# Optimization experiments

Measured on AMD Instinct MI355X. Metric: run time of the kernel, lower is better.

The kernel has to match this reference:

```python
import jax, jax.numpy as jnp
import numpy as np
import math

H = 4          # n_heads
LAM = 2.0      # gate_lambda
EPS = 1e-6


def _evid_gate(t, W, b):
    # t: [B,T,d] -> g: [B,T,1] via Normal-Inverse-Gamma evidential gate
    h = t @ W.T + b                                  # [B,T,4]
    mu, v_raw, a_raw, b_raw = jnp.split(h, 4, axis=-1)
    v = jax.nn.softplus(v_raw) + EPS
    alpha = jax.nn.softplus(a_raw) + 1.0 + EPS
    beta = jax.nn.softplus(b_raw) + EPS
    var_ep = beta / (v * (alpha - 1.0))
    g = jax.nn.sigmoid(mu) * jnp.exp(-LAM * var_ep)
    return jnp.maximum(g, 1e-6)


def _ln(t, g, b):
    m = jnp.mean(t, axis=-1, keepdims=True)
    v = jnp.var(t, axis=-1, keepdims=True)
    return (t - m) / jnp.sqrt(v + 1e-5) * g + b


def _split(t):
    B, T, d = t.shape
    return t.reshape(B, T, H, d // H).transpose(0, 2, 1, 3)  # [B,H,T,dk]


def _merge(t):
    B, h, T, dk = t.shape
    return t.transpose(0, 2, 1, 3).reshape(B, T, h * dk)


def _gated_attn(q, k, v, lg_q, lg_k, mask_k, dk):
    # q:[B,H,Tq,dk], k/v:[B,H,Tk,dk], lg_q:[B,Tq], lg_k:[B,Tk], mask_k:[B,Tk] bool
    s = jnp.einsum('bhqd,bhkd->bhqk', q, k) / math.sqrt(dk)
    s = s + lg_q[:, None, :, None] + lg_k[:, None, None, :]
    s = jnp.where(mask_k[:, None, None, :], s, -jnp.inf)
    a = jax.nn.softmax(s, axis=-1)                   # dropout is identity in eval
    return jnp.einsum('bhqk,bhkd->bhqd', a, v)


def setup_inputs():
    key = jax.random.key(0)
    ks = jax.random.split(key, 20)
    B, Nx, Ny, d = 16, 512, 1024, 256
    s = 0.02
    w = lambda k, shape: jax.random.normal(k, shape, jnp.float32) * s
    return {
        'x': jax.random.normal(ks[0], (B, Nx, d), jnp.float32),
        'y': jax.random.normal(ks[1], (B, Ny, d), jnp.float32),
        'x_mask': jnp.ones((B, Nx), bool),
        'y_mask': jnp.ones((B, Ny), bool),
        'Wqx': w(ks[2], (d, d)), 'Wkx': w(ks[3], (d, d)), 'Wvx': w(ks[4], (d, d)),
        'Wqy': w(ks[5], (d, d)), 'Wky': w(ks[6], (d, d)), 'Wvy': w(ks[7], (d, d)),
        'gWx': w(ks[8], (4, d)), 'gbx': jnp.zeros((4,), jnp.float32),
        'gWy': w(ks[9], (4, d)), 'gby': jnp.zeros((4,), jnp.float32),
        'Wox': w(ks[10], (d, d)), 'Woy': w(ks[11], (d, d)),
        'lnx_g': jnp.ones((d,), jnp.float32), 'lnx_b': jnp.zeros((d,), jnp.float32),
        'lny_g': jnp.ones((d,), jnp.float32), 'lny_b': jnp.zeros((d,), jnp.float32),
        'ffx_W': w(ks[12], (d, d)), 'ffx_b': jnp.zeros((d,), jnp.float32),
        'ffy_W': w(ks[13], (d, d)), 'ffy_b': jnp.zeros((d,), jnp.float32),
    }


def reference(x, y, x_mask, y_mask, Wqx, Wkx, Wvx, Wqy, Wky, Wvy,
              gWx, gbx, gWy, gby, Wox, Woy,
              lnx_g, lnx_b, lny_g, lny_b, ffx_W, ffx_b, ffy_W, ffy_b):
    d = x.shape[-1]
    dk = d // H
    qx, kx, vx = _split(x @ Wqx.T), _split(x @ Wkx.T), _split(x @ Wvx.T)
    qy, ky, vy = _split(y @ Wqy.T), _split(y @ Wky.T), _split(y @ Wvy.T)
    gx = _evid_gate(x, gWx, gbx)                     # [B,Nx,1]
    gy = _evid_gate(y, gWy, gby)                     # [B,Ny,1]
    lgx = jnp.log(gx)[..., 0]                        # [B,Nx]
    lgy = jnp.log(gy)[..., 0]                        # [B,Ny]

    out_x = _merge(_gated_attn(qx, ky, vy, lgx, lgy, y_mask, dk)) @ Wox.T
    x2 = _ln(x + out_x, lnx_g, lnx_b)
    x2 = _ln(x2 + jax.nn.silu(x2 @ ffx_W.T + ffx_b), lnx_g, lnx_b)

    out_y = _merge(_gated_attn(qy, kx, vx, lgy, lgx, x_mask, dk)) @ Woy.T
    y2 = _ln(y + out_y, lny_g, lny_b)
    y2 = _ln(y2 + jax.nn.silu(y2 @ ffy_W.T + ffy_b), lny_g, lny_b)

    return x2, y2, gx[..., 0], gy[..., 0]
```

## Files before the change

kernel.cpp:

```cpp
#include <hip/hip_runtime.h>
#include <stdint.h>

typedef unsigned short u16;
typedef unsigned int   u32;
typedef __attribute__((ext_vector_type(8))) short bf16x8;
typedef __attribute__((ext_vector_type(4))) float f32x4;

__device__ __forceinline__ u16 f2b(float f) {
    union { float f; u32 i; } v; v.f = f;
    return (u16)((v.i + 0x7fffu + ((v.i >> 16) & 1u)) >> 16);
}
__device__ __forceinline__ float b2f(u16 u) {
    union { float f; u32 i; } v; v.i = ((u32)u) << 16; return v.f;
}
__device__ __forceinline__ bf16x8 pack8(const float* s) {
    union { bf16x8 v; u16 u[8]; } r;
    #pragma unroll
    for (int i = 0; i < 8; i++) r.u[i] = f2b(s[i]);
    return r.v;
}
__device__ __forceinline__ float softplus_f(float x) {
    return x > 15.f ? x : log1pf(__expf(x));
}

__global__ __launch_bounds__(256) void prep(
    const float* __restrict__ X, const float* __restrict__ Y,
    const float* __restrict__ gWx, const float* __restrict__ gbx,
    const float* __restrict__ gWy, const float* __restrict__ gby,
    float* __restrict__ goutx, float* __restrict__ lgx,
    float* __restrict__ gouty, float* __restrict__ lgy,
    u16* __restrict__ xb, u16* __restrict__ yb,
    const float* p0, const float* p1, const float* p2, const float* p3,
    const float* p4, const float* p5, const float* p6, const float* p7,
    const float* p8, const float* p9, u16* __restrict__ wdst)
{
    const int blk = blockIdx.x;
    const int t = threadIdx.x;
    if (blk < 3072) {
        int g = blk * 256 + t;
        const bool isx = g < 262144;
        const float* src; u16* dst; size_t off; int tok;
        const float *gW, *gb; float *go, *lg;
        if (isx) {
            src = X; dst = xb; off = (size_t)g * 8; tok = g >> 5;
            gW = gWx; gb = gbx; go = goutx; lg = lgx;
        } else {
            int g2 = g - 262144;
            src = Y; dst = yb; off = (size_t)g2 * 8; tok = g2 >> 5;
            gW = gWy; gb = gby; go = gouty; lg = lgy;
        }
        float tmp[8];
        *(float4*)&tmp[0] = *(const float4*)(src + off);
        *(float4*)&tmp[4] = *(const float4*)(src + off + 4);
        *(bf16x8*)(dst + off) = pack8(tmp);

        const int c0 = (t & 31) * 8;
        float a[4];
        #pragma unroll
        for (int j = 0; j < 4; j++) {
            float4 w0 = *(const float4*)(gW + j * 256 + c0);
            float4 w1 = *(const float4*)(gW + j * 256 + c0 + 4);
            a[j] = tmp[0]*w0.x + tmp[1]*w0.y + tmp[2]*w0.z + tmp[3]*w0.w
                 + tmp[4]*w1.x + tmp[5]*w1.y + tmp[6]*w1.z + tmp[7]*w1.w;
        }
        #pragma unroll
        for (int o = 16; o > 0; o >>= 1) {
            #pragma unroll
            for (int j = 0; j < 4; j++) a[j] += __shfl_xor(a[j], o);
        }
        if ((t & 31) == 0) {
            float mu    = a[0] + gb[0];
            float v     = softplus_f(a[1] + gb[1]) + 1e-6f;
            float alpha = softplus_f(a[2] + gb[2]) + 1.0f + 1e-6f;
            float beta  = softplus_f(a[3] + gb[3]) + 1e-6f;
            float var_ep = beta / (v * (alpha - 1.0f));
            float sig = 1.0f / (1.0f + __expf(-mu));
            float gg = fmaxf(sig * __expf(-2.0f * var_ep), 1e-6f);
            go[tok] = gg;
            lg[tok] = log2f(gg);
        }
    } else {
        int g = (blk - 3072) * 256 + t;
        int wsel = g >> 13, off = g & 8191;
        const float* src;
        switch (wsel) {
            case 0: src = p0; break; case 1: src = p1; break;
            case 2: src = p2; break; case 3: src = p3; break;
            case 4: src = p4; break; case 5: src = p5; break;
            case 6: src = p6; break; case 7: src = p7; break;
            case 8: src = p8; break; default: src = p9; break;
        }
        float tmp[8];
        *(float4*)&tmp[0] = *(const float4*)(src + (size_t)off * 8);
        *(float4*)&tmp[4] = *(const float4*)(src + (size_t)off * 8 + 4);
        *(bf16x8*)(wdst + ((size_t)wsel * 65536) + (size_t)off * 8) = pack8(tmp);
    }
}

__global__ __launch_bounds__(256, 2) void gemm_qkv(
    const u16* __restrict__ Axb, const u16* __restrict__ Ayb,
    const u16* __restrict__ Wx, const u16* __restrict__ Wy,
    u16* __restrict__ Qx, u16* __restrict__ Kx, u16* __restrict__ VTx,
    u16* __restrict__ Qy, u16* __restrict__ Ky, u16* __restrict__ VTy)
{
    __shared__ short smem[2 * 128 * 72];
    short* As = smem;
    short* Ws = smem + 128 * 72;
    const int t = threadIdx.x;
    const int id = blockIdx.x;
    const int wk = (id & 7) * 144 + (id >> 3);
    const int bn = wk % 6;
    int bm = wk / 6;
    const bool isx = bm < 64;
    const u16* A  = isx ? Axb : Ayb;
    const u16* W  = isx ? Wx : Wy;
    u16* Qo  = isx ? Qx : Qy;
    u16* Ko  = isx ? Kx : Ky;
    u16* VTo = isx ? VTx : VTy;
    const int tqsh = isx ? 9 : 10;
    if (!isx) bm -= 64;

    const int w = t >> 6, lane = t & 63, li = lane & 15, quad = lane >> 4;
    const int wm = (w >> 1) * 64, wn = (w & 1) * 64;
    const int sr = t >> 1, scb = (t & 1) * 32;

    f32x4 zero = {0.f, 0.f, 0.f, 0.f};
    f32x4 acc[4][4];
    #pragma unroll
    for (int a = 0; a < 4; a++)
        #pragma unroll
        for (int b = 0; b < 4; b++) acc[a][b] = zero;

    for (int ch = 0; ch < 4; ch++) {
        const int k0 = ch * 64;
        if (ch) __syncthreads();
        {
            const u16* Ap = A + (size_t)(bm * 128 + sr) * 256 + k0 + scb;
            const u16* Wp = W + (size_t)(bn * 128 + sr) * 256 + k0 + scb;
            #pragma unroll
            for (int j = 0; j < 4; j++) {
                *(uint4*)&As[sr * 72 + scb + j * 8] = *(const uint4*)(Ap + j * 8);
                *(uint4*)&Ws[sr * 72 + scb + j * 8] = *(const uint4*)(Wp + j * 8);
            }
        }
        __syncthreads();
        #pragma unroll
        for (int c = 0; c < 2; c++) {
            bf16x8 af[4], bf[4];
            #pragma unroll
            for (int mt = 0; mt < 4; mt++)
                af[mt] = *(const bf16x8*)&As[(wm + mt * 16 + li) * 72 + c * 32 + quad * 8];
            #pragma unroll
            for (int nt = 0; nt < 4; nt++)
                bf[nt] = *(const bf16x8*)&Ws[(wn + nt * 16 + li) * 72 + c * 32 + quad * 8];
            #pragma unroll
            for (int mt = 0; mt < 4; mt++)
                #pragma unroll
                for (int nt = 0; nt < 4; nt++)
                    acc[mt][nt] = __builtin_amdgcn_mfma_f32_16x16x32_bf16(
                        af[mt], bf[nt], acc[mt][nt], 0, 0, 0);
        }
    }

    const int sel = bn >> 1;
    if (sel < 2) {
        u16* Co = (sel == 0) ? Qo : Ko;
        #pragma unroll
        for (int nt = 0; nt < 4; nt++) {
            const int c = (bn * 128 + wn + nt * 16 + li) & 255;
            #pragma unroll
            for (int mt = 0; mt < 4; mt++) {
                const int row0 = bm * 128 + wm + mt * 16 + quad * 4;
                #pragma unroll
                for (int i = 0; i < 4; i++)
                    Co[(size_t)(row0 + i) * 256 + c] = f2b(acc[mt][nt][i]);
            }
        }
    } else {
        __syncthreads();
        short* Trans = smem;
        #pragma unroll
        for (int nt = 0; nt < 4; nt++) {
            const int cl = wn + nt * 16 + li;
            #pragma unroll
            for (int mt = 0; mt < 4; mt++) {
                const int rl0 = wm + mt * 16 + quad * 4;
                #pragma unroll
                for (int i = 0; i < 4; i++)
                    Trans[cl * 136 + rl0 + i] = (short)f2b(acc[mt][nt][i]);
            }
        }
        __syncthreads();
        const int dl = t >> 1, seg = t & 1;
        const int col = (bn - 4) * 128 + dl;
        const int h = col >> 6, dd = col & 63;
        const int bz = (bm * 128) >> tqsh;
        const int key0 = (bm * 128) & ((1 << tqsh) - 1);
        u16* dst = VTo + ((((size_t)(bz * 4 + h)) * 64 + dd) << tqsh) + key0 + seg * 64;
        #pragma unroll
        for (int k = 0; k < 8; k++)
            *(uint4*)(dst + k * 8) = *(const uint4*)&Trans[dl * 136 + seg * 64 + k * 8];
    }
}

__global__ __launch_bounds__(256, 3) void attn3(
    const u16* __restrict__ Q1, const u16* __restrict__ K1, const u16* __restrict__ VT1,
    const float* __restrict__ LG1, u16* __restrict__ O1,
    const u16* __restrict__ Q2, const u16* __restrict__ K2, const u16* __restrict__ VT2,
    const float* __restrict__ LG2, u16* __restrict__ O2)
{
    __shared__ short Ks[64][72];
    __shared__ short VTs[64][72];
    __shared__ short Ps[128][72];
    __shared__ float Lk[64];

    const int t = threadIdx.x;
    const int id = blockIdx.x;
    const int wk = (id & 7) * 96 + (id >> 3);
    const int xi = wk % 12;
    const int rest = wk / 12;
    const int h = rest & 3;
    const int bz = rest >> 2;
    const bool ph1 = xi < 4;
    const int qtl = ph1 ? xi : xi - 4;
    const u16* Q  = ph1 ? Q1 : Q2;
    const u16* K  = ph1 ? K1 : K2;
    const u16* VT = ph1 ? VT1 : VT2;
    const float* LG = ph1 ? LG1 : LG2;
    u16* O = ph1 ? O1 : O2;
    const int Tq = ph1 ? 512 : 1024;
    const int Tk = ph1 ? 1024 : 512;

    const int w = t >> 6, lane = t & 63, li = lane & 15, quad = lane >> 4;
    const int q0 = qtl * 128;

    bf16x8 qf[2][2];
    #pragma unroll
    for (int s = 0; s < 2; s++) {
        const u16* qp = Q + (size_t)(bz * Tq + q0 + s * 64 + w * 16 + li) * 256 + h * 64 + quad * 8;
        qf[s][0] = *(const bf16x8*)qp;
        qf[s][1] = *(const bf16x8*)(qp + 32);
    }

    float lsum[2] = {0.f, 0.f};
    f32x4 zero = {0.f, 0.f, 0.f, 0.f};
    f32x4 oacc[2][4];
    #pragma unroll
    for (int s = 0; s < 2; s++)
        #pragma unroll
        for (int md = 0; md < 4; md++) oacc[s][md] = zero;

    const int sr = t >> 2, sc = (t & 3) * 16;
    const u16* Kp  = K + (size_t)(bz * Tk + sr) * 256 + h * 64 + sc;
    const u16* VTp = VT + ((size_t)(bz * 4 + h) * 64 + sr) * Tk + sc;
    const float* LGp = LG + (size_t)bz * Tk;

    uint4 pk0, pk1, pv0, pv1;
    float plk;
    pk0 = *(const uint4*)(Kp);
    pk1 = *(const uint4*)(Kp + 8);
    pv0 = *(const uint4*)(VTp);
    pv1 = *(const uint4*)(VTp + 8);
    plk = (t < 64) ? LGp[t] : 0.f;

    const float SCL = 0.18033688f;

    for (int kt = 0; kt < Tk; kt += 64) {
        __syncthreads();
        *(uint4*)&Ks[sr][sc]      = pk0;
        *(uint4*)&Ks[sr][sc + 8]  = pk1;
        *(uint4*)&VTs[sr][sc]     = pv0;
        *(uint4*)&VTs[sr][sc + 8] = pv1;
        if (t < 64) Lk[t] = plk;
        __syncthreads();
        if (kt + 64 < Tk) {
            pk0 = *(const uint4*)(Kp + (size_t)(kt + 64) * 256);
            pk1 = *(const uint4*)(Kp + (size_t)(kt + 64) * 256 + 8);
            pv0 = *(const uint4*)(VTp + kt + 64);
            pv1 = *(const uint4*)(VTp + kt + 64 + 8);
            if (t < 64) plk = LGp[kt + 64 + t];
        }

        #pragma unroll
        for (int s = 0; s < 2; s++) {
            f32x4 sacc[4] = {zero, zero, zero, zero};
            #pragma unroll
            for (int c = 0; c < 2; c++)
                #pragma unroll
                for (int mt = 0; mt < 4; mt++) {
                    bf16x8 af = *(const bf16x8*)&Ks[mt * 16 + li][c * 32 + quad * 8];
                    sacc[mt] = __builtin_amdgcn_mfma_f32_16x16x32_bf16(af, qf[s][c], sacc[mt], 0, 0, 0);
                }
            #pragma unroll
            for (int mt = 0; mt < 4; mt++) {
                float4 lk4 = *(const float4*)&Lk[mt * 16 + quad * 4];
                float x0 = fmaf(sacc[mt][0], SCL, lk4.x);
                float x1 = fmaf(sacc[mt][1], SCL, lk4.y);
                float x2 = fmaf(sacc[mt][2], SCL, lk4.z);
                float x3 = fmaf(sacc[mt][3], SCL, lk4.w);
                float p0, p1, p2, p3;
                asm("v_exp_f32 %0, %1" : "=v"(p0) : "v"(x0));
                asm("v_exp_f32 %0, %1" : "=v"(p1) : "v"(x1));
                asm("v_exp_f32 %0, %1" : "=v"(p2) : "v"(x2));
                asm("v_exp_f32 %0, %1" : "=v"(p3) : "v"(x3));
                lsum[s] += (p0 + p1) + (p2 + p3);
                u32 lo, hi;
                asm("v_cvt_pk_bf16_f32 %0, %1, %2" : "=v"(lo) : "v"(p0), "v"(p1));
                asm("v_cvt_pk_bf16_f32 %0, %1, %2" : "=v"(hi) : "v"(p2), "v"(p3));
                uint2 st; st.x = lo; st.y = hi;
                *(uint2*)&Ps[s * 64 + w * 16 + li][mt * 16 + quad * 4] = st;
            }
        }

        #pragma unroll
        for (int c = 0; c < 2; c++) {
            bf16x8 vf[4], pf[2];
            #pragma unroll
            for (int md = 0; md < 4; md++)
                vf[md] = *(const bf16x8*)&VTs[md * 16 + li][c * 32 + quad * 8];
            #pragma unroll
            for (int s = 0; s < 2; s++)
                pf[s] = *(const bf16x8*)&Ps[s * 64 + w * 16 + li][c * 32 + quad * 8];
            #pragma unroll
            for (int s = 0; s < 2; s++)
                #pragma unroll
                for (int md = 0; md < 4; md++)
                    oacc[s][md] = __builtin_amdgcn_mfma_f32_16x16x32_bf16(
                        vf[md], pf[s], oacc[s][md], 0, 0, 0);
        }
    }

    #pragma unroll
    for (int s = 0; s < 2; s++) {
        float l = lsum[s];
        l += __shfl_xor(l, 16);
        l += __shfl_xor(l, 32);
        const float inv = 1.0f / l;
        u16* op = O + (size_t)(bz * Tq + q0 + s * 64 + w * 16 + li) * 256 + h * 64;
        #pragma unroll
        for (int md = 0; md < 4; md++) {
            float o0 = oacc[s][md][0] * inv;
            float o1 = oacc[s][md][1] * inv;
            float o2 = oacc[s][md][2] * inv;
            float o3 = oacc[s][md][3] * inv;
            u32 lo, hi;
            asm("v_cvt_pk_bf16_f32 %0, %1, %2" : "=v"(lo) : "v"(o0), "v"(o1));
            asm("v_cvt_pk_bf16_f32 %0, %1, %2" : "=v"(hi) : "v"(o2), "v"(o3));
            uint2 st; st.x = lo; st.y = hi;
            *(uint2*)(op + md * 16 + quad * 4) = st;
        }
    }
}

template<int ACT>
__global__ __launch_bounds__(256, 3) void gemm_ln(
    const u16* __restrict__ Axb, const u16* __restrict__ Ayb,
    const u16* __restrict__ Wxb, const u16* __restrict__ Wyb,
    const float* __restrict__ bx, const float* __restrict__ by,
    const float* __restrict__ Rx, const float* __restrict__ Ry,
    const float* __restrict__ gxv, const float* __restrict__ bxv,
    const float* __restrict__ gyv, const float* __restrict__ byv,
    float* __restrict__ Fx, float* __restrict__ Fy,
    u16* __restrict__ Bx, u16* __restrict__ By)
{
    __shared__ short As[32 * 72];
    __shared__ short Ws[256 * 72];
    __shared__ float Sred[32][4];
    __shared__ float Ssq[32][4];

    const int t = threadIdx.x;
    int blk = blockIdx.x;
    const bool isx = blk < 256;
    const u16* A = isx ? Axb : Ayb;
    const u16* W = isx ? Wxb : Wyb;
    const float* bias  = isx ? bx : by;
    const float* RES   = isx ? Rx : Ry;
    const float* gamma = isx ? gxv : gyv;
    const float* beta  = isx ? bxv : byv;
    float* F = isx ? Fx : Fy;
    u16*   B = isx ? Bx : By;
    if (!isx) blk -= 256;
    const int r0 = blk * 32;

    const int w = t >> 6, lane = t & 63, li = lane & 15, quad = lane >> 4;
    const int wn = w * 64;

    f32x4 zero = {0.f, 0.f, 0.f, 0.f};
    f32x4 acc[2][4];
    #pragma unroll
    for (int a = 0; a < 2; a++)
        #pragma unroll
        for (int b = 0; b < 4; b++) acc[a][b] = zero;

    const int asr = t >> 3, asc = (t & 7) * 8;
    const int wr0 = t >> 3, wseg = (t & 7) * 8;
    for (int ch = 0; ch < 4; ch++) {
        const int k0 = ch * 64;
        if (ch) __syncthreads();
        {
            *(uint4*)&As[asr * 72 + asc] =
                *(const uint4*)(A + (size_t)(r0 + asr) * 256 + k0 + asc);
            #pragma unroll
            for (int jj = 0; jj < 8; jj++) {
                const int row = wr0 + jj * 32;
                *(uint4*)&Ws[row * 72 + wseg] =
                    *(const uint4*)(W + (size_t)row * 256 + k0 + wseg);
            }
        }
        __syncthreads();
        #pragma unroll
        for (int c = 0; c < 2; c++) {
            bf16x8 af[2], bf[4];
            #pragma unroll
            for (int mt = 0; mt < 2; mt++)
                af[mt] = *(const bf16x8*)&As[(mt * 16 + li) * 72 + c * 32 + quad * 8];
            #pragma unroll
            for (int nt = 0; nt < 4; nt++)
                bf[nt] = *(const bf16x8*)&Ws[(wn + nt * 16 + li) * 72 + c * 32 + quad * 8];
            #pragma unroll
            for (int mt = 0; mt < 2; mt++)
                #pragma unroll
                for (int nt = 0; nt < 4; nt++)
                    acc[mt][nt] = __builtin_amdgcn_mfma_f32_16x16x32_bf16(
                        af[mt], bf[nt], acc[mt][nt], 0, 0, 0);
        }
    }

    float bv[4], gv[4], btv[4];
    #pragma unroll
    for (int nt = 0; nt < 4; nt++) {
        const int col = wn + nt * 16 + li;
        bv[nt]  = bias ? bias[col] : 0.f;
        gv[nt]  = gamma[col];
        btv[nt] = beta[col];
    }
    float psum[2][4], psq[2][4];
    #pragma unroll
    for (int mt = 0; mt < 2; mt++) {
        #pragma unroll
        for (int i = 0; i < 4; i++) { psum[mt][i] = 0.f; psq[mt][i] = 0.f; }
        #pragma unroll
        for (int nt = 0; nt < 4; nt++) {
            const int col = wn + nt * 16 + li;
            #pragma unroll
            for (int i = 0; i < 4; i++) {
                float v = acc[mt][nt][i] + bv[nt];
                if (ACT) v = v / (1.f + __expf(-v));
                const int row = mt * 16 + quad * 4 + i;
                v += RES[(size_t)(r0 + row) * 256 + col];
                acc[mt][nt][i] = v;
                psum[mt][i] += v;
                psq[mt][i]  += v * v;
            }
        }
        #pragma unroll
        for (int i = 0; i < 4; i++) {
            #pragma unroll
            for (int off = 1; off < 16; off <<= 1) {
                psum[mt][i] += __shfl_xor(psum[mt][i], off);
                psq[mt][i]  += __shfl_xor(psq[mt][i], off);
            }
        }
    }
    if (li == 0) {
        #pragma unroll
        for (int mt = 0; mt < 2; mt++)
            #pragma unroll
            for (int i = 0; i < 4; i++) {
                Sred[mt * 16 + quad * 4 + i][w] = psum[mt][i];
                Ssq[mt * 16 + quad * 4 + i][w]  = psq[mt][i];
            }
    }
    __syncthreads();
    #pragma unroll
    for (int mt = 0; mt < 2; mt++) {
        #pragma unroll
        for (int i = 0; i < 4; i++) {
            const int row = mt * 16 + quad * 4 + i;
            float4 s4 = *(const float4*)&Sred[row][0];
            float4 q4 = *(const float4*)&Ssq[row][0];
            float S  = (s4.x + s4.y) + (s4.z + s4.w);
            float S2 = (q4.x + q4.y) + (q4.z + q4.w);
            float mean = S * (1.0f / 256.0f);
            float var  = S2 * (1.0f / 256.0f) - mean * mean;
            float rstd = rsqrtf(var + 1e-5f);
            #pragma unroll
            for (int nt = 0; nt < 4; nt++) {
                const int col = wn + nt * 16 + li;
                float outv = (acc[mt][nt][i] - mean) * rstd * gv[nt] + btv[nt];
                F[(size_t)(r0 + row) * 256 + col] = outv;
                if (B) B[(size_t)(r0 + row) * 256 + col] = f2b(outv);
            }
        }
    }
}

extern "C" void kernel_launch(void* const* d_in, const int* in_sizes, int n_in,
                              void* d_out, int out_size, void* d_ws, size_t ws_size,
                              hipStream_t stream)
{
    const float* x = (const float*)d_in[0];
    const float* y = (const float*)d_in[1];
    const int wb = (n_in >= 24) ? 4 : 2;
    const float* Wqx  = (const float*)d_in[wb + 0];
    const float* Wkx  = (const float*)d_in[wb + 1];
    const float* Wvx  = (const float*)d_in[wb + 2];
    const float* Wqy  = (const float*)d_in[wb + 3];
    const float* Wky  = (const float*)d_in[wb + 4];
    const float* Wvy  = (const float*)d_in[wb + 5];
    const float* gWx  = (const float*)d_in[wb + 6];
    const float* gbx  = (const float*)d_in[wb + 7];
    const float* gWy  = (const float*)d_in[wb + 8];
    const float* gby  = (const float*)d_in[wb + 9];
    const float* Wox  = (const float*)d_in[wb + 10];
    const float* Woy  = (const float*)d_in[wb + 11];
    const float* lnxg = (const float*)d_in[wb + 12];
    const float* lnxb = (const float*)d_in[wb + 13];
    const float* lnyg = (const float*)d_in[wb + 14];
    const float* lnyb = (const float*)d_in[wb + 15];
    const float* ffxW = (const float*)d_in[wb + 16];
    const float* ffxb = (const float*)d_in[wb + 17];
    const float* ffyW = (const float*)d_in[wb + 18];
    const float* ffyb = (const float*)d_in[wb + 19];

    char* ws = (char*)d_ws;
    float* lgx = (float*)(ws);
    float* lgy = (float*)(ws + 32768);
    u16* wbf   = (u16*)(ws + 98304);
    u16* xbf   = (u16*)(ws + 1409024);
    u16* ybf   = xbf + (size_t)8192 * 256;
    u16* qb    = ybf + (size_t)16384 * 256;
    u16* kb    = qb  + (size_t)8192 * 256;
    u16* vtb   = kb  + (size_t)16384 * 256;
    u16* qb2   = vtb + (size_t)16384 * 256;
    u16* kb2   = qb2 + (size_t)16384 * 256;
    u16* vtb2  = kb2 + (size_t)8192 * 256;
    u16* ctxx  = vtb2 + (size_t)8192 * 256;
    u16* ctxy  = ctxx + (size_t)8192 * 256;
    u16* xa    = ctxy + (size_t)16384 * 256;
    u16* ya    = xa + (size_t)8192 * 256;

    float* out_x2 = (float*)d_out;
    float* out_y2 = out_x2 + 2097152;
    float* out_gx = out_x2 + 6291456;
    float* out_gy = out_x2 + 6299648;

    prep<<<3392, 256, 0, stream>>>(
        x, y, gWx, gbx, gWy, gby, out_gx, lgx, out_gy, lgy,
        xbf, ybf,
        Wqx, Wkx, Wvx, Wqy, Wky, Wvy, Wox, Woy, ffxW, ffyW, wbf);
    gemm_qkv<<<dim3(1152), 256, 0, stream>>>(
        xbf, ybf, wbf + 0 * 65536, wbf + 3 * 65536,
        qb, kb2, vtb2, qb2, kb, vtb);
    attn3<<<dim3(768), 256, 0, stream>>>(
        qb, kb, vtb, lgy, ctxx, qb2, kb2, vtb2, lgx, ctxy);
    gemm_ln<0><<<768, 256, 0, stream>>>(
        ctxx, ctxy, wbf + 6 * 65536, wbf + 7 * 65536,
        nullptr, nullptr, x, y,
        lnxg, lnxb, lnyg, lnyb, out_x2, out_y2, xa, ya);
    gemm_ln<1><<<768, 256, 0, stream>>>(
        xa, ya, wbf + 8 * 65536, wbf + 9 * 65536,
        ffxb, ffyb, out_x2, out_y2,
        lnxg, lnxb, lnyg, lnyb, out_x2, out_y2, nullptr, nullptr);

    (void)in_sizes; (void)out_size; (void)ws_size;
}
```

Before: 210.3 us.

## Fuse output projection LN and feed-forward LN into one GEMM kernel

Merges the two gemm_ln launches into a single kernel. The first LayerNorm result stays in registers and is staged as bf16 in shared memory, and the second GEMM (the FFN weight) consumes it there. The SiLU, residual and second LayerNorm are then applied before writing. This removes one launch, the fp32 write and re-read of the intermediate output, and the bf16 activation round trip through global memory. In exchange, each block now runs two GEMMs serially, uses more shared memory, and the occupancy hint drops from 3 to 2 blocks.

```diff
diff --git a/kernel.cpp b/kernel.cpp
--- a/kernel.cpp
+++ b/kernel.cpp
@@ -352,33 +352,33 @@
     }
 }
 
-template<int ACT>
-__global__ __launch_bounds__(256, 3) void gemm_ln(
+__global__ __launch_bounds__(256, 2) void gemm_ffln(
     const u16* __restrict__ Axb, const u16* __restrict__ Ayb,
-    const u16* __restrict__ Wxb, const u16* __restrict__ Wyb,
-    const float* __restrict__ bx, const float* __restrict__ by,
+    const u16* __restrict__ W1x, const u16* __restrict__ W1y,
+    const u16* __restrict__ W2x, const u16* __restrict__ W2y,
+    const float* __restrict__ fbx, const float* __restrict__ fby,
     const float* __restrict__ Rx, const float* __restrict__ Ry,
     const float* __restrict__ gxv, const float* __restrict__ bxv,
     const float* __restrict__ gyv, const float* __restrict__ byv,
-    float* __restrict__ Fx, float* __restrict__ Fy,
-    u16* __restrict__ Bx, u16* __restrict__ By)
+    float* __restrict__ Fx, float* __restrict__ Fy)
 {
     __shared__ short As[32 * 72];
     __shared__ short Ws[256 * 72];
+    __shared__ short A2[32 * 264];
     __shared__ float Sred[32][4];
     __shared__ float Ssq[32][4];
 
     const int t = threadIdx.x;
     int blk = blockIdx.x;
     const bool isx = blk < 256;
-    const u16* A = isx ? Axb : Ayb;
-    const u16* W = isx ? Wxb : Wyb;
-    const float* bias  = isx ? bx : by;
+    const u16* A  = isx ? Axb : Ayb;
+    const u16* W1 = isx ? W1x : W1y;
+    const u16* W2 = isx ? W2x : W2y;
+    const float* fb    = isx ? fbx : fby;
     const float* RES   = isx ? Rx : Ry;
     const float* gamma = isx ? gxv : gyv;
     const float* beta  = isx ? bxv : byv;
     float* F = isx ? Fx : Fy;
-    u16*   B = isx ? Bx : By;
     if (!isx) blk -= 256;
     const int r0 = blk * 32;
 
@@ -394,6 +394,7 @@
 
     const int asr = t >> 3, asc = (t & 7) * 8;
     const int wr0 = t >> 3, wseg = (t & 7) * 8;
+
     for (int ch = 0; ch < 4; ch++) {
         const int k0 = ch * 64;
         if (ch) __syncthreads();
@@ -404,7 +405,7 @@
             for (int jj = 0; jj < 8; jj++) {
                 const int row = wr0 + jj * 32;
                 *(uint4*)&Ws[row * 72 + wseg] =
-                    *(const uint4*)(W + (size_t)row * 256 + k0 + wseg);
+                    *(const uint4*)(W1 + (size_t)row * 256 + k0 + wseg);
             }
         }
         __syncthreads();
@@ -426,14 +427,15 @@
         }
     }
 
-    float bv[4], gv[4], btv[4];
+    float gv[4], btv[4], fbv[4];
     #pragma unroll
     for (int nt = 0; nt < 4; nt++) {
         const int col = wn + nt * 16 + li;
-        bv[nt]  = bias ? bias[col] : 0.f;
         gv[nt]  = gamma[col];
         btv[nt] = beta[col];
-    }
+        fbv[nt] = fb[col];
+    }
+
     float psum[2][4], psq[2][4];
     #pragma unroll
     for (int mt = 0; mt < 2; mt++) {
@@ -444,10 +446,8 @@
             const int col = wn + nt * 16 + li;
             #pragma unroll
             for (int i = 0; i < 4; i++) {
-                float v = acc[mt][nt][i] + bv[nt];
-                if (ACT) v = v / (1.f + __expf(-v));
                 const int row = mt * 16 + quad * 4 + i;
-                v += RES[(size_t)(r0 + row) * 256 + col];
+                float v = acc[mt][nt][i] + RES[(size_t)(r0 + row) * 256 + col];
                 acc[mt][nt][i] = v;
                 psum[mt][i] += v;
                 psq[mt][i]  += v * v;
@@ -472,6 +472,7 @@
             }
     }
     __syncthreads();
+
     #pragma unroll
     for (int mt = 0; mt < 2; mt++) {
         #pragma unroll
@@ -487,9 +488,102 @@
             #pragma unroll
             for (int nt = 0; nt < 4; nt++) {
                 const int col = wn + nt * 16 + li;
-                float outv = (acc[mt][nt][i] - mean) * rstd * gv[nt] + btv[nt];
-                F[(size_t)(r0 + row) * 256 + col] = outv;
-                if (B) B[(size_t)(r0 + row) * 256 + col] = f2b(outv);
+                float ln = (acc[mt][nt][i] - mean) * rstd * gv[nt] + btv[nt];
+                acc[mt][nt][i] = ln;
+                A2[row * 264 + col] = (short)f2b(ln);
+            }
+        }
+    }
+
+    f32x4 acc2[2][4];
+    #pragma unroll
+    for (int a = 0; a < 2; a++)
+        #pragma unroll
+        for (int b = 0; b < 4; b++) acc2[a][b] = zero;
+
+    for (int ch = 0; ch < 4; ch++) {
+        const int k0 = ch * 64;
+        __syncthreads();
+        {
+            #pragma unroll
+            for (int jj = 0; jj < 8; jj++) {
+                const int row = wr0 + jj * 32;
+                *(uint4*)&Ws[row * 72 + wseg] =
+                    *(const uint4*)(W2 + (size_t)row * 256 + k0 + wseg);
+            }
+        }
+        __syncthreads();
+        #pragma unroll
+        for (int c = 0; c < 2; c++) {
+            bf16x8 af[2], bf[4];
+            #pragma unroll
+            for (int mt = 0; mt < 2; mt++)
+                af[mt] = *(const bf16x8*)&A2[(mt * 16 + li) * 264 + k0 + c * 32 + quad * 8];
+            #pragma unroll
+            for (int nt = 0; nt < 4; nt++)
+                bf[nt] = *(const bf16x8*)&Ws[(wn + nt * 16 + li) * 72 + c * 32 + quad * 8];
+            #pragma unroll
+            for (int mt = 0; mt < 2; mt++)
+                #pragma unroll
+                for (int nt = 0; nt < 4; nt++)
+                    acc2[mt][nt] = __builtin_amdgcn_mfma_f32_16x16x32_bf16(
+                        af[mt], bf[nt], acc2[mt][nt], 0, 0, 0);
+        }
+    }
+
+    #pragma unroll
+    for (int mt = 0; mt < 2; mt++) {
+        #pragma unroll
+        for (int i = 0; i < 4; i++) { psum[mt][i] = 0.f; psq[mt][i] = 0.f; }
+        #pragma unroll
+        for (int nt = 0; nt < 4; nt++) {
+            #pragma unroll
+            for (int i = 0; i < 4; i++) {
+                float u = acc2[mt][nt][i] + fbv[nt];
+                u = u / (1.f + __expf(-u));
+                u += acc[mt][nt][i];
+                acc2[mt][nt][i] = u;
+                psum[mt][i] += u;
+                psq[mt][i]  += u * u;
+            }
+        }
+        #pragma unroll
+        for (int i = 0; i < 4; i++) {
+            #pragma unroll
+            for (int off = 1; off < 16; off <<= 1) {
+                psum[mt][i] += __shfl_xor(psum[mt][i], off);
+                psq[mt][i]  += __shfl_xor(psq[mt][i], off);
+            }
+        }
+    }
+    if (li == 0) {
+        #pragma unroll
+        for (int mt = 0; mt < 2; mt++)
+            #pragma unroll
+            for (int i = 0; i < 4; i++) {
+                Sred[mt * 16 + quad * 4 + i][w] = psum[mt][i];
+                Ssq[mt * 16 + quad * 4 + i][w]  = psq[mt][i];
+            }
+    }
+    __syncthreads();
+
+    #pragma unroll
+    for (int mt = 0; mt < 2; mt++) {
+        #pragma unroll
+        for (int i = 0; i < 4; i++) {
+            const int row = mt * 16 + quad * 4 + i;
+            float4 s4 = *(const float4*)&Sred[row][0];
+            float4 q4 = *(const float4*)&Ssq[row][0];
+            float S  = (s4.x + s4.y) + (s4.z + s4.w);
+            float S2 = (q4.x + q4.y) + (q4.z + q4.w);
+            float mean = S * (1.0f / 256.0f);
+            float var  = S2 * (1.0f / 256.0f) - mean * mean;
+            float rstd = rsqrtf(var + 1e-5f);
+            #pragma unroll
+            for (int nt = 0; nt < 4; nt++) {
+                const int col = wn + nt * 16 + li;
+                F[(size_t)(r0 + row) * 256 + col] =
+                    (acc2[mt][nt][i] - mean) * rstd * gv[nt] + btv[nt];
             }
         }
     }
@@ -537,8 +631,6 @@
     u16* vtb2  = kb2 + (size_t)8192 * 256;
     u16* ctxx  = vtb2 + (size_t)8192 * 256;
     u16* ctxy  = ctxx + (size_t)8192 * 256;
-    u16* xa    = ctxy + (size_t)16384 * 256;
-    u16* ya    = xa + (size_t)8192 * 256;
 
     float* out_x2 = (float*)d_out;
     float* out_y2 = out_x2 + 2097152;
@@ -554,14 +646,11 @@
         qb, kb2, vtb2, qb2, kb, vtb);
     attn3<<<dim3(768), 256, 0, stream>>>(
         qb, kb, vtb, lgy, ctxx, qb2, kb2, vtb2, lgx, ctxy);
-    gemm_ln<0><<<768, 256, 0, stream>>>(
+    gemm_ffln<<<768, 256, 0, stream>>>(
         ctxx, ctxy, wbf + 6 * 65536, wbf + 7 * 65536,
-        nullptr, nullptr, x, y,
-        lnxg, lnxb, lnyg, lnyb, out_x2, out_y2, xa, ya);
-    gemm_ln<1><<<768, 256, 0, stream>>>(
-        xa, ya, wbf + 8 * 65536, wbf + 9 * 65536,
-        ffxb, ffyb, out_x2, out_y2,
-        lnxg, lnxb, lnyg, lnyb, out_x2, out_y2, nullptr, nullptr);
+        wbf + 8 * 65536, wbf + 9 * 65536,
+        ffxb, ffyb, x, y,
+        lnxg, lnxb, lnyg, lnyb, out_x2, out_y2);
 
     (void)in_sizes; (void)out_size; (void)ws_size;
 }
```

Measured after the change: 209.3 us. About the same (-0.5%).
